# Kernel optimization log

Measured on AMD Instinct MI355X. Metric: run time of the kernel, lower is better.

## Reference

```python
import jax, jax.numpy as jnp
import numpy as np

N_NODES = 100000
N_EDGES = 3200000
N_GRAPHS = 64
IN_DIM = 64
LATENT = 64
DIST_STD = 1.0


def _gcn_conv(x, W, b, src, dst, dinv):
    """PyG GCNConv: out = D^-1/2 (A+I) D^-1/2 (x W) + b, with dinv = deg^-1/2."""
    n = x.shape[0]
    h = x @ W  # [N, out]
    coef = dinv[src] * dinv[dst]  # per-edge norm
    agg = jax.ops.segment_sum(h[src] * coef[:, None], dst, num_segments=n)
    # self-loop contribution with norm dinv[i]^2
    return agg + h * (dinv * dinv)[:, None] + b


def _mean_pool(x, batch, num_graphs):
    sums = jax.ops.segment_sum(x, batch, num_segments=num_graphs)
    cnts = jax.ops.segment_sum(jnp.ones((x.shape[0],), x.dtype), batch, num_segments=num_graphs)
    return sums / jnp.maximum(cnts, 1.0)[:, None]


def setup_inputs() -> dict:
    key = jax.random.key(0)
    ks = jax.random.split(key, 12)
    x = jax.random.normal(ks[0], (N_NODES, IN_DIM), jnp.float32)
    edge_index = jax.random.randint(ks[1], (2, N_EDGES), 0, N_NODES, jnp.int64 if jax.config.jax_enable_x64 else jnp.int32).astype(jnp.int32)
    batch = jnp.sort(jax.random.randint(ks[2], (N_NODES,), 0, N_GRAPHS)).astype(jnp.int32)

    def glorot(k, shape):
        fan_in, fan_out = shape
        s = jnp.sqrt(6.0 / (fan_in + fan_out))
        return jax.random.uniform(k, shape, jnp.float32, -s, s)

    return {
        "x": x, "edge_index": edge_index, "batch": batch,
        "W1m": glorot(ks[3], (IN_DIM, 16)), "b1m": jnp.zeros((16,), jnp.float32),
        "W2m": glorot(ks[4], (16, 32)), "b2m": jnp.zeros((32,), jnp.float32),
        "W3m": glorot(ks[5], (32, LATENT)), "b3m": jnp.zeros((LATENT,), jnp.float32),
        "W1l": glorot(ks[6], (IN_DIM, 16)), "b1l": jnp.zeros((16,), jnp.float32),
        "W2l": glorot(ks[7], (16, 32)), "b2l": jnp.zeros((32,), jnp.float32),
        "W3l": glorot(ks[8], (32, LATENT)), "b3l": jnp.zeros((LATENT,), jnp.float32),
        "Wfc": glorot(ks[9], (LATENT, 160000)), "bfc": jnp.zeros((160000,), jnp.float32),
        "eps": jax.random.normal(ks[10], (N_GRAPHS, LATENT), jnp.float32) * DIST_STD,
    }


def reference(x, edge_index, batch, W1m, b1m, W2m, b2m, W3m, b3m,
              W1l, b1l, W2l, b2l, W3l, b3l, Wfc, bfc, eps):
    src, dst = edge_index[0], edge_index[1]
    n = x.shape[0]
    # degrees include self-loop (+1)
    deg = jax.ops.segment_sum(jnp.ones((src.shape[0],), x.dtype), dst, num_segments=n) + 1.0
    dinv = jax.lax.rsqrt(deg)

    mu = jax.nn.relu(_gcn_conv(x, W1m, b1m, src, dst, dinv))
    mu = jax.nn.relu(_gcn_conv(mu, W2m, b2m, src, dst, dinv))
    mu = jax.nn.relu(_gcn_conv(mu, W3m, b3m, src, dst, dinv))
    mu = _mean_pool(mu, batch, N_GRAPHS)

    log = jax.nn.relu(_gcn_conv(x, W1l, b1l, src, dst, dinv))
    log = jax.nn.relu(_gcn_conv(log, W2l, b2l, src, dst, dinv))
    log = jax.nn.relu(_gcn_conv(log, W3l, b3l, src, dst, dinv))
    logvar = _mean_pool(log, batch, N_GRAPHS)

    # latent sample (training mode): z = mu + eps * exp(0.5*logvar)
    z = mu + eps * jnp.exp(0.5 * logvar)

    # decode: sigmoid(z Wfc + bfc) -> [G, 400, 400]
    output = jax.nn.sigmoid(z @ Wfc + bfc).reshape(-1, 400, 400)
    return output, mu, logvar
```

## Files before the change

kernel.cpp:

```cpp
#include <hip/hip_runtime.h>
#include <hip/hip_bf16.h>

#define N_NODES 100000
#define N_EDGES 3200000
#define N_GRAPHS 64
#define NB 391
#define KCH 8192
#define NCHUNK ((N_EDGES + KCH - 1) / KCH)
#define MAXBKT 10240

__device__ __forceinline__ void atomAddF(float* p, float v) {
    unsafeAtomicAdd(p, v);
}

__device__ __forceinline__ float lo2f(unsigned u) { return __uint_as_float(u << 16); }
__device__ __forceinline__ float hi2f(unsigned u) { return __uint_as_float(u & 0xFFFF0000u); }
__device__ __forceinline__ unsigned pack2(float a, float b) {
    unsigned ha = __bfloat16_as_ushort(__float2bfloat16(a));
    unsigned hb = __bfloat16_as_ushort(__float2bfloat16(b));
    return ha | (hb << 16);
}

__global__ __launch_bounds__(512) void k_binCount(const int* __restrict__ dst,
                                                  int* __restrict__ gcount) {
    __shared__ int hist[NB];
    for (int t = threadIdx.x; t < NB; t += 512) hist[t] = 0;
    __syncthreads();
    int base = blockIdx.x * KCH;
    int cnt = min(KCH, N_EDGES - base);
    for (int i = threadIdx.x; i < cnt; i += 512)
        atomicAdd(&hist[dst[base + i] >> 8], 1);
    __syncthreads();
    for (int t = threadIdx.x; t < NB; t += 512)
        if (hist[t]) atomicAdd(&gcount[t], hist[t]);
}

__global__ __launch_bounds__(512) void k_scanB(const int* __restrict__ gcount,
                                               int* __restrict__ gbase,
                                               int* __restrict__ gcursor,
                                               int* __restrict__ rowptr) {
    __shared__ int s[512];
    int v = (threadIdx.x < NB) ? gcount[threadIdx.x] : 0;
    s[threadIdx.x] = v;
    __syncthreads();
    for (int off = 1; off < 512; off <<= 1) {
        int t = (threadIdx.x >= off) ? s[threadIdx.x - off] : 0;
        __syncthreads();
        s[threadIdx.x] += t;
        __syncthreads();
    }
    if (threadIdx.x < NB) {
        int e = s[threadIdx.x] - v;
        gbase[threadIdx.x] = e;
        gcursor[threadIdx.x] = e;
    }
    if (threadIdx.x == 0) rowptr[N_NODES] = N_EDGES;
}

__global__ __launch_bounds__(512) void k_binA(const int* __restrict__ src,
                                              const int* __restrict__ dst,
                                              int* __restrict__ gcursor,
                                              int* __restrict__ binned) {
    __shared__ int hist[512];
    __shared__ int sc[512];
    __shared__ int sexc[512];
    __shared__ int rbase[512];
    __shared__ int stage[KCH];
    hist[threadIdx.x] = 0;
    __syncthreads();
    int base = blockIdx.x * KCH;
    int cnt = min(KCH, N_EDGES - base);
    int myb[16], mypos[16];
    int nmine = 0;
    for (int i = 0; i < 16; ++i) {
        int idx = i * 512 + threadIdx.x;
        if (idx < cnt) {
            int b = dst[base + idx] >> 8;
            myb[nmine] = b;
            mypos[nmine] = atomicAdd(&hist[b], 1);
            ++nmine;
        }
    }
    __syncthreads();
    int v = hist[threadIdx.x];
    sc[threadIdx.x] = v;
    __syncthreads();
    for (int off = 1; off < 512; off <<= 1) {
        int t = (threadIdx.x >= off) ? sc[threadIdx.x - off] : 0;
        __syncthreads();
        sc[threadIdx.x] += t;
        __syncthreads();
    }
    sexc[threadIdx.x] = sc[threadIdx.x] - v;
    __syncthreads();
    if (threadIdx.x < NB && v > 0)
        rbase[threadIdx.x] = atomicAdd(&gcursor[threadIdx.x], v);
    for (int k = 0; k < nmine; ++k) {
        int e = base + k * 512 + threadIdx.x;
        int p = ((dst[e] & 255) << 24) | src[e];
        stage[sexc[myb[k]] + mypos[k]] = p;
    }
    __syncthreads();
    for (int j = threadIdx.x; j < cnt; j += 512) {
        int lo = 0, hi = NB - 1;
        while (lo < hi) {
            int mid = (lo + hi + 1) >> 1;
            if (sexc[mid] <= j) lo = mid; else hi = mid - 1;
        }
        binned[rbase[lo] + (j - sexc[lo])] = stage[j];
    }
}

__global__ __launch_bounds__(512) void k_passB(const int* __restrict__ gbase,
                                               int* __restrict__ csr,
                                               int* __restrict__ rowptr,
                                               float* __restrict__ dinv) {
    int b = blockIdx.x;
    int rb = gbase[b];
    int re = (b == NB - 1) ? N_EDGES : gbase[b + 1];
    int cnt = re - rb;
    int nbase = b << 8;
    int nn = min(nbase + 256, N_NODES) - nbase;
    __shared__ int stage[MAXBKT];
    __shared__ int nhist[256];
    __shared__ int sc[256];
    __shared__ int ncur[256];
    for (int t = threadIdx.x; t < 256; t += 512) nhist[t] = 0;
    __syncthreads();
    for (int j = threadIdx.x; j < cnt; j += 512) {
        int p = csr[rb + j];
        stage[j] = p;
        atomicAdd(&nhist[((unsigned)p) >> 24], 1);
    }
    __syncthreads();
    if (threadIdx.x < 256) sc[threadIdx.x] = nhist[threadIdx.x];
    __syncthreads();
    for (int off = 1; off < 256; off <<= 1) {
        int t = (threadIdx.x < 256 && threadIdx.x >= off) ? sc[threadIdx.x - off] : 0;
        __syncthreads();
        if (threadIdx.x < 256) sc[threadIdx.x] += t;
        __syncthreads();
    }
    if (threadIdx.x < 256) {
        int e = sc[threadIdx.x] - nhist[threadIdx.x];
        ncur[threadIdx.x] = e;
        if (threadIdx.x < nn) {
            rowptr[nbase + threadIdx.x] = rb + e;
            dinv[nbase + threadIdx.x] = rsqrtf((float)nhist[threadIdx.x] + 1.0f);
        }
    }
    __syncthreads();
    for (int j = threadIdx.x; j < cnt; j += 512) {
        int p = stage[j];
        int slot = atomicAdd(&ncur[((unsigned)p) >> 24], 1);
        csr[rb + slot] = p;
    }
}

template<int LOGW, bool BIAS_RELU, bool OB, bool PRE>
__global__ void __launch_bounds__(256) k_gatherB(
        const int* __restrict__ rowptr, const int* __restrict__ csr,
        const unsigned* __restrict__ in ,
        const float* __restrict__ dinv,
        const float* __restrict__ ba, const float* __restrict__ bb,
        void* __restrict__ out) {
    constexpr int W4 = (1 << LOGW) / 4;
    constexpr int NPB = 256 / W4;
    int n = blockIdx.x * NPB + (threadIdx.x / W4);
    int sub = threadIdx.x % W4;
    const uint2* in2 = (const uint2*)in;
    uint2 u = in2[(size_t)n * W4 + sub];
    float4 acc = make_float4(lo2f(u.x), hi2f(u.x), lo2f(u.y), hi2f(u.y));
    int j = rowptr[n], end = rowptr[n + 1];
    for (; j + 4 <= end; j += 4) {
        int s0 = csr[j] & 0xFFFFFF;
        int s1 = csr[j + 1] & 0xFFFFFF;
        int s2 = csr[j + 2] & 0xFFFFFF;
        int s3 = csr[j + 3] & 0xFFFFFF;
        uint2 v0 = in2[(size_t)s0 * W4 + sub];
        uint2 v1 = in2[(size_t)s1 * W4 + sub];
        uint2 v2 = in2[(size_t)s2 * W4 + sub];
        uint2 v3 = in2[(size_t)s3 * W4 + sub];
        acc.x += (lo2f(v0.x) + lo2f(v1.x)) + (lo2f(v2.x) + lo2f(v3.x));
        acc.y += (hi2f(v0.x) + hi2f(v1.x)) + (hi2f(v2.x) + hi2f(v3.x));
        acc.z += (lo2f(v0.y) + lo2f(v1.y)) + (lo2f(v2.y) + lo2f(v3.y));
        acc.w += (hi2f(v0.y) + hi2f(v1.y)) + (hi2f(v2.y) + hi2f(v3.y));
    }
    for (; j < end; ++j) {
        int s = csr[j] & 0xFFFFFF;
        uint2 v = in2[(size_t)s * W4 + sub];
        acc.x += lo2f(v.x);
        acc.y += hi2f(v.x);
        acc.z += lo2f(v.y);
        acc.w += hi2f(v.y);
    }
    float di = dinv[n];
    acc.x *= di; acc.y *= di; acc.z *= di; acc.w *= di;
    if (BIAS_RELU) {
        constexpr int H = (1 << LOGW) / 2;
        int d = sub * 4;
        const float* bp = (d < H) ? (ba + d) : (bb + d - H);
        acc.x = fmaxf(acc.x + bp[0], 0.0f);
        acc.y = fmaxf(acc.y + bp[1], 0.0f);
        acc.z = fmaxf(acc.z + bp[2], 0.0f);
        acc.w = fmaxf(acc.w + bp[3], 0.0f);
    }
    if (PRE) {
        acc.x *= di; acc.y *= di; acc.z *= di; acc.w *= di;
    }
    if (OB) {
        ((uint2*)out)[(size_t)n * W4 + sub] =
            make_uint2(pack2(acc.x, acc.y), pack2(acc.z, acc.w));
    } else {
        ((float4*)out)[(size_t)n * W4 + sub] = acc;
    }
}

template<int IN_W, int OUT_HALF, int A_OFF, int A_W, int B_OFF, bool BR, bool OB, bool DS>
__global__ void k_dense4(const float* __restrict__ in,
                         const float* __restrict__ Wa, const float* __restrict__ ba,
                         const float* __restrict__ Wb, const float* __restrict__ bb,
                         const float* __restrict__ dinv,
                         void* __restrict__ out) {
    __shared__ float sWa[A_W * OUT_HALF];
    __shared__ float sWb[A_W * OUT_HALF];
    __shared__ float sba[OUT_HALF];
    __shared__ float sbb[OUT_HALF];
    for (int t = threadIdx.x; t < A_W * OUT_HALF; t += 256) {
        sWa[t] = Wa[t];
        sWb[t] = Wb[t];
    }
    if (BR && threadIdx.x < OUT_HALF) {
        sba[threadIdx.x] = ba[threadIdx.x];
        sbb[threadIdx.x] = bb[threadIdx.x];
    }
    __syncthreads();
    constexpr int TPN = OUT_HALF / 2;
    int idx = blockIdx.x * 256 + threadIdx.x;
    int n = idx / TPN;
    int q = idx % TPN;
    bool isB = (q * 4) >= OUT_HALF;
    int dd = q * 4 - (isB ? OUT_HALF : 0);
    const float* sW = isB ? sWb : sWa;
    int ko = isB ? B_OFF : A_OFF;
    float4 acc;
    if (BR) {
        const float* bp = isB ? (sbb + dd) : (sba + dd);
        acc = make_float4(bp[0], bp[1], bp[2], bp[3]);
    } else {
        acc = make_float4(0.f, 0.f, 0.f, 0.f);
    }
    const float* row = in + (size_t)n * IN_W + ko;
    #pragma unroll
    for (int k = 0; k < A_W; ++k) {
        float r = row[k];
        float4 wv = *(const float4*)&sW[k * OUT_HALF + dd];
        acc.x = fmaf(r, wv.x, acc.x);
        acc.y = fmaf(r, wv.y, acc.y);
        acc.z = fmaf(r, wv.z, acc.z);
        acc.w = fmaf(r, wv.w, acc.w);
    }
    if (BR) {
        acc.x = fmaxf(acc.x, 0.f); acc.y = fmaxf(acc.y, 0.f);
        acc.z = fmaxf(acc.z, 0.f); acc.w = fmaxf(acc.w, 0.f);
    }
    if (DS) {
        float dn = dinv[n];
        acc.x *= dn; acc.y *= dn; acc.z *= dn; acc.w *= dn;
    }
    if (OB) {
        ((uint2*)out)[idx] = make_uint2(pack2(acc.x, acc.y), pack2(acc.z, acc.w));
    } else {
        ((float4*)out)[idx] = acc;
    }
}

__global__ void k_pool2(const float* __restrict__ h3, const int* __restrict__ batch,
                        float* __restrict__ pool, int* __restrict__ cnt) {
    int g = blockIdx.x >> 2;
    int q = blockIdx.x & 3;
    __shared__ int sb[2];
    if (threadIdx.x < 2) {
        int target = g + threadIdx.x;
        int lo = 0, hi = N_NODES;
        while (lo < hi) {
            int mid = (lo + hi) >> 1;
            if (batch[mid] < target) lo = mid + 1; else hi = mid;
        }
        sb[threadIdx.x] = lo;
    }
    __syncthreads();
    int start = sb[0], end = sb[1];
    int d = threadIdx.x & 127;
    int half = threadIdx.x >> 7;
    float acc = 0.0f;
    for (int n = start + q * 2 + half; n < end; n += 8)
        acc += h3[(size_t)n * 128 + d];
    __shared__ float sred[256];
    sred[threadIdx.x] = acc;
    __syncthreads();
    if (half == 0)
        atomAddF(&pool[g * 128 + d], sred[threadIdx.x] + sred[threadIdx.x + 128]);
    if (threadIdx.x == 0 && q == 0) cnt[g] = end - start;
}

__global__ void k_final(const float* __restrict__ pool, const int* __restrict__ cnt,
                        const float* __restrict__ eps, float* __restrict__ zbuf,
                        float* __restrict__ out_mu, float* __restrict__ out_lv) {
    int idx = blockIdx.x * 256 + threadIdx.x;
    int g = idx >> 6;
    float c = fmaxf((float)cnt[g], 1.0f);
    float mu = pool[g * 128 + (idx & 63)] / c;
    float lv = pool[g * 128 + 64 + (idx & 63)] / c;
    zbuf[idx] = mu + eps[idx] * __expf(0.5f * lv);
    out_mu[idx] = mu;
    out_lv[idx] = lv;
}

__global__ void __launch_bounds__(256) k_decode(const float* __restrict__ zbuf,
                                                const float* __restrict__ Wfc,
                                                const float* __restrict__ bfc,
                                                float* __restrict__ out) {
    __shared__ float sz[64 * 64];
    for (int t = threadIdx.x; t < 4096; t += 256) sz[t] = zbuf[t];
    __syncthreads();
    int j = blockIdx.x * 256 + threadIdx.x;
    float bias = bfc[j];
    float acc[64];
    #pragma unroll
    for (int g = 0; g < 64; ++g) acc[g] = bias;
    #pragma unroll 4
    for (int k4 = 0; k4 < 16; ++k4) {
        float w0 = Wfc[(k4 * 4 + 0) * 160000 + j];
        float w1 = Wfc[(k4 * 4 + 1) * 160000 + j];
        float w2 = Wfc[(k4 * 4 + 2) * 160000 + j];
        float w3 = Wfc[(k4 * 4 + 3) * 160000 + j];
        #pragma unroll
        for (int g = 0; g < 64; ++g) {
            float4 zv = *(const float4*)&sz[g * 64 + k4 * 4];
            acc[g] = fmaf(zv.x, w0, acc[g]);
            acc[g] = fmaf(zv.y, w1, acc[g]);
            acc[g] = fmaf(zv.z, w2, acc[g]);
            acc[g] = fmaf(zv.w, w3, acc[g]);
        }
    }
    #pragma unroll
    for (int g = 0; g < 64; ++g) {
        float s = 1.0f / (1.0f + __expf(-acc[g]));
        out[g * 160000 + j] = s;
    }
}

extern "C" void kernel_launch(void* const* d_in, const int* in_sizes, int n_in,
                              void* d_out, int out_size, void* d_ws, size_t ws_size,
                              hipStream_t stream) {
    const float* x     = (const float*)d_in[0];
    const int*   ei    = (const int*)d_in[1];
    const int*   batch = (const int*)d_in[2];
    const float *W1m = (const float*)d_in[3],  *b1m = (const float*)d_in[4];
    const float *W2m = (const float*)d_in[5],  *b2m = (const float*)d_in[6];
    const float *W3m = (const float*)d_in[7],  *b3m = (const float*)d_in[8];
    const float *W1l = (const float*)d_in[9],  *b1l = (const float*)d_in[10];
    const float *W2l = (const float*)d_in[11], *b2l = (const float*)d_in[12];
    const float *W3l = (const float*)d_in[13], *b3l = (const float*)d_in[14];
    const float *Wfc = (const float*)d_in[15], *bfc = (const float*)d_in[16];
    const float *eps = (const float*)d_in[17];

    const int* srcv = ei;
    const int* dstv = ei + N_EDGES;

    char* w = (char*)d_ws;
    auto alloc = [&](size_t bytes) -> char* {
        char* p = w;
        w += (bytes + 255) & ~(size_t)255;
        return p;
    };
    int*   gcount = (int*)  alloc((size_t)NB * 4);
    int*   gbase  = (int*)  alloc((size_t)NB * 4);
    int*   gcursor= (int*)  alloc((size_t)NB * 4);
    int*   rowptr = (int*)  alloc((size_t)(N_NODES + 1) * 4);
    float* dinv   = (float*)alloc((size_t)N_NODES * 4);
    float* pool   = (float*)alloc((size_t)N_GRAPHS * 128 * 4);
    int*   cnt    = (int*)  alloc((size_t)N_GRAPHS * 4);
    float* zbuf   = (float*)alloc((size_t)N_GRAPHS * 64 * 4);
    float* arena = (float*)alloc((size_t)N_NODES * 192 * 4);
    float* A   = arena;
    float* B   = arena + (size_t)N_NODES * 64;
    int*   csr = (int*)(arena + (size_t)N_NODES * 128);
    float* h3  = B;

    float* out    = (float*)d_out;
    float* out_mu = out + 10240000;
    float* out_lv = out + 10240000 + 4096;

    hipMemsetAsync(gcount, 0, (size_t)NB * 4, stream);
    hipMemsetAsync(pool, 0, (size_t)N_GRAPHS * 128 * 4, stream);

    k_binCount<<<NCHUNK, 512, 0, stream>>>(dstv, gcount);
    k_scanB<<<1, 512, 0, stream>>>(gcount, gbase, gcursor, rowptr);
    k_binA<<<NCHUNK, 512, 0, stream>>>(srcv, dstv, gcursor, csr);
    k_passB<<<NB, 512, 0, stream>>>(gbase, csr, rowptr, dinv);

    k_dense4<64, 16, 0, 64, 0, false, true, true><<<N_NODES * 8 / 256, 256, 0, stream>>>(
        x, W1m, b1m, W1l, b1l, dinv, A);
    k_gatherB<5, true, true, true><<<N_NODES / 32, 256, 0, stream>>>(
        rowptr, csr, (const unsigned*)A, dinv, b1m, b1l, B);

    k_gatherB<5, false, false, false><<<N_NODES / 32, 256, 0, stream>>>(
        rowptr, csr, (const unsigned*)B, dinv, b1m, b1l, A);
    k_dense4<32, 32, 0, 16, 16, true, true, true><<<N_NODES * 16 / 256, 256, 0, stream>>>(
        A, W2m, b2m, W2l, b2l, dinv, B);

    k_gatherB<6, false, false, false><<<N_NODES / 16, 256, 0, stream>>>(
        rowptr, csr, (const unsigned*)B, dinv, b1m, b1l, A);
    k_dense4<64, 64, 0, 32, 32, true, false, false><<<N_NODES * 32 / 256, 256, 0, stream>>>(
        A, W3m, b3m, W3l, b3l, dinv, h3);

    k_pool2<<<N_GRAPHS * 4, 256, 0, stream>>>(h3, batch, pool, cnt);
    k_final<<<16, 256, 0, stream>>>(pool, cnt, eps, zbuf, out_mu, out_lv);

    k_decode<<<625, 256, 0, stream>>>(zbuf, Wfc, bfc, out);
}
```

Before: 513.7 us.

## Fuse layer-3 dense with mean pooling, simplify edge binning, unroll gather

The layer-3 dense transform is fused with mean pooling, so the per-node layer-3 output is no longer written and read back. Per-graph counts now come from a binary search in the final kernel. Edge binning scatters directly to global memory through an intermediate binned buffer instead of staging and scanning in shared memory, and passB reads from that buffer. The binCount loads are vectorised to int4 and the gather loop is unrolled by 8 for more memory-level parallelism. The trade-offs are less coalesced scatter writes in binning and more atomics in pooling.

Result: slower. 533.0 us (+3.8%).

```diff
diff --git a/kernel.cpp b/kernel.cpp
--- a/kernel.cpp
+++ b/kernel.cpp
@@ -7,7 +7,6 @@
 #define NB 391
 #define KCH 8192
 #define NCHUNK ((N_EDGES + KCH - 1) / KCH)
-#define MAXBKT 10240
 
 __device__ __forceinline__ void atomAddF(float* p, float v) {
     unsafeAtomicAdd(p, v);
@@ -28,8 +27,14 @@
     __syncthreads();
     int base = blockIdx.x * KCH;
     int cnt = min(KCH, N_EDGES - base);
-    for (int i = threadIdx.x; i < cnt; i += 512)
-        atomicAdd(&hist[dst[base + i] >> 8], 1);
+    const int4* d4 = (const int4*)(dst + base);
+    for (int i = threadIdx.x; i < cnt / 4; i += 512) {
+        int4 v = d4[i];
+        atomicAdd(&hist[v.x >> 8], 1);
+        atomicAdd(&hist[v.y >> 8], 1);
+        atomicAdd(&hist[v.z >> 8], 1);
+        atomicAdd(&hist[v.w >> 8], 1);
+    }
     __syncthreads();
     for (int t = threadIdx.x; t < NB; t += 512)
         if (hist[t]) atomicAdd(&gcount[t], hist[t]);
@@ -62,56 +67,40 @@
                                               int* __restrict__ gcursor,
                                               int* __restrict__ binned) {
     __shared__ int hist[512];
-    __shared__ int sc[512];
-    __shared__ int sexc[512];
     __shared__ int rbase[512];
-    __shared__ int stage[KCH];
     hist[threadIdx.x] = 0;
     __syncthreads();
     int base = blockIdx.x * KCH;
     int cnt = min(KCH, N_EDGES - base);
     int myb[16], mypos[16];
-    int nmine = 0;
+    #pragma unroll
     for (int i = 0; i < 16; ++i) {
         int idx = i * 512 + threadIdx.x;
         if (idx < cnt) {
             int b = dst[base + idx] >> 8;
-            myb[nmine] = b;
-            mypos[nmine] = atomicAdd(&hist[b], 1);
-            ++nmine;
+            myb[i] = b;
+            mypos[i] = atomicAdd(&hist[b], 1);
+        } else {
+            myb[i] = -1;
         }
     }
     __syncthreads();
     int v = hist[threadIdx.x];
-    sc[threadIdx.x] = v;
-    __syncthreads();
-    for (int off = 1; off < 512; off <<= 1) {
-        int t = (threadIdx.x >= off) ? sc[threadIdx.x - off] : 0;
-        __syncthreads();
-        sc[threadIdx.x] += t;
-        __syncthreads();
-    }
-    sexc[threadIdx.x] = sc[threadIdx.x] - v;
-    __syncthreads();
     if (threadIdx.x < NB && v > 0)
         rbase[threadIdx.x] = atomicAdd(&gcursor[threadIdx.x], v);
-    for (int k = 0; k < nmine; ++k) {
-        int e = base + k * 512 + threadIdx.x;
-        int p = ((dst[e] & 255) << 24) | src[e];
-        stage[sexc[myb[k]] + mypos[k]] = p;
-    }
-    __syncthreads();
-    for (int j = threadIdx.x; j < cnt; j += 512) {
-        int lo = 0, hi = NB - 1;
-        while (lo < hi) {
-            int mid = (lo + hi + 1) >> 1;
-            if (sexc[mid] <= j) lo = mid; else hi = mid - 1;
+    __syncthreads();
+    #pragma unroll
+    for (int i = 0; i < 16; ++i) {
+        if (myb[i] >= 0) {
+            int e = base + i * 512 + threadIdx.x;
+            int p = ((dst[e] & 255) << 24) | src[e];
+            binned[rbase[myb[i]] + mypos[i]] = p;
         }
-        binned[rbase[lo] + (j - sexc[lo])] = stage[j];
     }
 }
 
 __global__ __launch_bounds__(512) void k_passB(const int* __restrict__ gbase,
+                                               const int* __restrict__ binned,
                                                int* __restrict__ csr,
                                                int* __restrict__ rowptr,
                                                float* __restrict__ dinv) {
@@ -121,17 +110,13 @@
     int cnt = re - rb;
     int nbase = b << 8;
     int nn = min(nbase + 256, N_NODES) - nbase;
-    __shared__ int stage[MAXBKT];
     __shared__ int nhist[256];
     __shared__ int sc[256];
     __shared__ int ncur[256];
     for (int t = threadIdx.x; t < 256; t += 512) nhist[t] = 0;
     __syncthreads();
-    for (int j = threadIdx.x; j < cnt; j += 512) {
-        int p = csr[rb + j];
-        stage[j] = p;
-        atomicAdd(&nhist[((unsigned)p) >> 24], 1);
-    }
+    for (int j = threadIdx.x; j < cnt; j += 512)
+        atomicAdd(&nhist[((unsigned)binned[rb + j]) >> 24], 1);
     __syncthreads();
     if (threadIdx.x < 256) sc[threadIdx.x] = nhist[threadIdx.x];
     __syncthreads();
@@ -151,7 +136,7 @@
     }
     __syncthreads();
     for (int j = threadIdx.x; j < cnt; j += 512) {
-        int p = stage[j];
+        int p = binned[rb + j];
         int slot = atomicAdd(&ncur[((unsigned)p) >> 24], 1);
         csr[rb + slot] = p;
     }
@@ -172,7 +157,33 @@
     uint2 u = in2[(size_t)n * W4 + sub];
     float4 acc = make_float4(lo2f(u.x), hi2f(u.x), lo2f(u.y), hi2f(u.y));
     int j = rowptr[n], end = rowptr[n + 1];
-    for (; j + 4 <= end; j += 4) {
+    for (; j + 8 <= end; j += 8) {
+        int s0 = csr[j] & 0xFFFFFF;
+        int s1 = csr[j + 1] & 0xFFFFFF;
+        int s2 = csr[j + 2] & 0xFFFFFF;
+        int s3 = csr[j + 3] & 0xFFFFFF;
+        int s4 = csr[j + 4] & 0xFFFFFF;
+        int s5 = csr[j + 5] & 0xFFFFFF;
+        int s6 = csr[j + 6] & 0xFFFFFF;
+        int s7 = csr[j + 7] & 0xFFFFFF;
+        uint2 v0 = in2[(size_t)s0 * W4 + sub];
+        uint2 v1 = in2[(size_t)s1 * W4 + sub];
+        uint2 v2 = in2[(size_t)s2 * W4 + sub];
+        uint2 v3 = in2[(size_t)s3 * W4 + sub];
+        uint2 v4 = in2[(size_t)s4 * W4 + sub];
+        uint2 v5 = in2[(size_t)s5 * W4 + sub];
+        uint2 v6 = in2[(size_t)s6 * W4 + sub];
+        uint2 v7 = in2[(size_t)s7 * W4 + sub];
+        acc.x += ((lo2f(v0.x) + lo2f(v1.x)) + (lo2f(v2.x) + lo2f(v3.x)))
+               + ((lo2f(v4.x) + lo2f(v5.x)) + (lo2f(v6.x) + lo2f(v7.x)));
+        acc.y += ((hi2f(v0.x) + hi2f(v1.x)) + (hi2f(v2.x) + hi2f(v3.x)))
+               + ((hi2f(v4.x) + hi2f(v5.x)) + (hi2f(v6.x) + hi2f(v7.x)));
+        acc.z += ((lo2f(v0.y) + lo2f(v1.y)) + (lo2f(v2.y) + lo2f(v3.y)))
+               + ((lo2f(v4.y) + lo2f(v5.y)) + (lo2f(v6.y) + lo2f(v7.y)));
+        acc.w += ((hi2f(v0.y) + hi2f(v1.y)) + (hi2f(v2.y) + hi2f(v3.y)))
+               + ((hi2f(v4.y) + hi2f(v5.y)) + (hi2f(v6.y) + hi2f(v7.y)));
+    }
+    if (j + 4 <= end) {
         int s0 = csr[j] & 0xFFFFFF;
         int s1 = csr[j + 1] & 0xFFFFFF;
         int s2 = csr[j + 2] & 0xFFFFFF;
@@ -185,6 +196,7 @@
         acc.y += (hi2f(v0.x) + hi2f(v1.x)) + (hi2f(v2.x) + hi2f(v3.x));
         acc.z += (lo2f(v0.y) + lo2f(v1.y)) + (lo2f(v2.y) + lo2f(v3.y));
         acc.w += (hi2f(v0.y) + hi2f(v1.y)) + (hi2f(v2.y) + hi2f(v3.y));
+        j += 4;
     }
     for (; j < end; ++j) {
         int s = csr[j] & 0xFFFFFF;
@@ -275,41 +287,87 @@
     }
 }
 
-__global__ void k_pool2(const float* __restrict__ h3, const int* __restrict__ batch,
-                        float* __restrict__ pool, int* __restrict__ cnt) {
-    int g = blockIdx.x >> 2;
-    int q = blockIdx.x & 3;
-    __shared__ int sb[2];
-    if (threadIdx.x < 2) {
-        int target = g + threadIdx.x;
+__global__ void __launch_bounds__(256) k_dense3pool(
+        const float* __restrict__ in,
+        const float* __restrict__ Wa, const float* __restrict__ ba,
+        const float* __restrict__ Wb, const float* __restrict__ bb,
+        const int* __restrict__ batch,
+        float* __restrict__ pool) {
+    __shared__ float sWa[32 * 64];
+    __shared__ float sWb[32 * 64];
+    __shared__ float sba[64];
+    __shared__ float sbb[64];
+    __shared__ float sacc[2][128];
+    for (int t = threadIdx.x; t < 32 * 64; t += 256) {
+        sWa[t] = Wa[t];
+        sWb[t] = Wb[t];
+    }
+    if (threadIdx.x < 64) {
+        sba[threadIdx.x] = ba[threadIdx.x];
+        sbb[threadIdx.x] = bb[threadIdx.x];
+    }
+    sacc[0][threadIdx.x & 127] = 0.0f;
+    sacc[1][threadIdx.x & 127] = 0.0f;
+    __syncthreads();
+    int idx = blockIdx.x * 256 + threadIdx.x;
+    int n = idx / 32;
+    int q = idx % 32;
+    bool isB = q >= 16;
+    int dd = q * 4 - (isB ? 64 : 0);
+    const float* sW = isB ? sWb : sWa;
+    const float* bp = isB ? (sbb + dd) : (sba + dd);
+    float4 acc = make_float4(bp[0], bp[1], bp[2], bp[3]);
+    const float* row = in + (size_t)n * 64 + (isB ? 32 : 0);
+    #pragma unroll
+    for (int k = 0; k < 32; ++k) {
+        float r = row[k];
+        float4 wv = *(const float4*)&sW[k * 64 + dd];
+        acc.x = fmaf(r, wv.x, acc.x);
+        acc.y = fmaf(r, wv.y, acc.y);
+        acc.z = fmaf(r, wv.z, acc.z);
+        acc.w = fmaf(r, wv.w, acc.w);
+    }
+    acc.x = fmaxf(acc.x, 0.f); acc.y = fmaxf(acc.y, 0.f);
+    acc.z = fmaxf(acc.z, 0.f); acc.w = fmaxf(acc.w, 0.f);
+    int g0 = batch[blockIdx.x * 8];
+    int gn = batch[n];
+    int gsel = gn - g0;
+    int d = q * 4;
+    if (gsel <= 1) {
+        atomicAdd(&sacc[gsel][d + 0], acc.x);
+        atomicAdd(&sacc[gsel][d + 1], acc.y);
+        atomicAdd(&sacc[gsel][d + 2], acc.z);
+        atomicAdd(&sacc[gsel][d + 3], acc.w);
+    } else {
+        atomAddF(&pool[gn * 128 + d + 0], acc.x);
+        atomAddF(&pool[gn * 128 + d + 1], acc.y);
+        atomAddF(&pool[gn * 128 + d + 2], acc.z);
+        atomAddF(&pool[gn * 128 + d + 3], acc.w);
+    }
+    __syncthreads();
+    int gs = threadIdx.x >> 7;
+    int dj = threadIdx.x & 127;
+    float v = sacc[gs][dj];
+    if (v != 0.0f) atomAddF(&pool[(g0 + gs) * 128 + dj], v);
+}
+
+__global__ void k_final(const float* __restrict__ pool, const int* __restrict__ batch,
+                        const float* __restrict__ eps, float* __restrict__ zbuf,
+                        float* __restrict__ out_mu, float* __restrict__ out_lv) {
+    int idx = blockIdx.x * 256 + threadIdx.x;
+    int g = idx >> 6;
+    int bounds[2];
+    #pragma unroll
+    for (int t = 0; t < 2; ++t) {
+        int target = g + t;
         int lo = 0, hi = N_NODES;
         while (lo < hi) {
             int mid = (lo + hi) >> 1;
             if (batch[mid] < target) lo = mid + 1; else hi = mid;
         }
-        sb[threadIdx.x] = lo;
-    }
-    __syncthreads();
-    int start = sb[0], end = sb[1];
-    int d = threadIdx.x & 127;
-    int half = threadIdx.x >> 7;
-    float acc = 0.0f;
-    for (int n = start + q * 2 + half; n < end; n += 8)
-        acc += h3[(size_t)n * 128 + d];
-    __shared__ float sred[256];
-    sred[threadIdx.x] = acc;
-    __syncthreads();
-    if (half == 0)
-        atomAddF(&pool[g * 128 + d], sred[threadIdx.x] + sred[threadIdx.x + 128]);
-    if (threadIdx.x == 0 && q == 0) cnt[g] = end - start;
-}
-
-__global__ void k_final(const float* __restrict__ pool, const int* __restrict__ cnt,
-                        const float* __restrict__ eps, float* __restrict__ zbuf,
-                        float* __restrict__ out_mu, float* __restrict__ out_lv) {
-    int idx = blockIdx.x * 256 + threadIdx.x;
-    int g = idx >> 6;
-    float c = fmaxf((float)cnt[g], 1.0f);
+        bounds[t] = lo;
+    }
+    float c = fmaxf((float)(bounds[1] - bounds[0]), 1.0f);
     float mu = pool[g * 128 + (idx & 63)] / c;
     float lv = pool[g * 128 + 64 + (idx & 63)] / c;
     zbuf[idx] = mu + eps[idx] * __expf(0.5f * lv);
@@ -381,13 +439,12 @@
     int*   rowptr = (int*)  alloc((size_t)(N_NODES + 1) * 4);
     float* dinv   = (float*)alloc((size_t)N_NODES * 4);
     float* pool   = (float*)alloc((size_t)N_GRAPHS * 128 * 4);
-    int*   cnt    = (int*)  alloc((size_t)N_GRAPHS * 4);
     float* zbuf   = (float*)alloc((size_t)N_GRAPHS * 64 * 4);
     float* arena = (float*)alloc((size_t)N_NODES * 192 * 4);
-    float* A   = arena;
-    float* B   = arena + (size_t)N_NODES * 64;
-    int*   csr = (int*)(arena + (size_t)N_NODES * 128);
-    float* h3  = B;
+    float* A      = arena;
+    float* B      = arena + (size_t)N_NODES * 64;
+    int*   csr    = (int*)(arena + (size_t)N_NODES * 128);
+    int*   binned = (int*)(arena + (size_t)N_NODES * 160);
 
     float* out    = (float*)d_out;
     float* out_mu = out + 10240000;
@@ -398,8 +455,8 @@
 
     k_binCount<<<NCHUNK, 512, 0, stream>>>(dstv, gcount);
     k_scanB<<<1, 512, 0, stream>>>(gcount, gbase, gcursor, rowptr);
-    k_binA<<<NCHUNK, 512, 0, stream>>>(srcv, dstv, gcursor, csr);
-    k_passB<<<NB, 512, 0, stream>>>(gbase, csr, rowptr, dinv);
+    k_binA<<<NCHUNK, 512, 0, stream>>>(srcv, dstv, gcursor, binned);
+    k_passB<<<NB, 512, 0, stream>>>(gbase, binned, csr, rowptr, dinv);
 
     k_dense4<64, 16, 0, 64, 0, false, true, true><<<N_NODES * 8 / 256, 256, 0, stream>>>(
         x, W1m, b1m, W1l, b1l, dinv, A);
@@ -413,11 +470,10 @@
 
     k_gatherB<6, false, false, false><<<N_NODES / 16, 256, 0, stream>>>(
         rowptr, csr, (const unsigned*)B, dinv, b1m, b1l, A);
-    k_dense4<64, 64, 0, 32, 32, true, false, false><<<N_NODES * 32 / 256, 256, 0, stream>>>(
-        A, W3m, b3m, W3l, b3l, dinv, h3);
-
-    k_pool2<<<N_GRAPHS * 4, 256, 0, stream>>>(h3, batch, pool, cnt);
-    k_final<<<16, 256, 0, stream>>>(pool, cnt, eps, zbuf, out_mu, out_lv);
+    k_dense3pool<<<N_NODES * 32 / 256, 256, 0, stream>>>(
+        A, W3m, b3m, W3l, b3l, batch, pool);
+
+    k_final<<<16, 256, 0, stream>>>(pool, batch, eps, zbuf, out_mu, out_lv);
 
     k_decode<<<625, 256, 0, stream>>>(zbuf, Wfc, bfc, out);
 }
```
